# Kernel tuning notes

Measured on AMD Instinct MI355X. Metric: run time of the kernel, lower is better.

## Reference

```python
import jax, jax.numpy as jnp
import numpy as np

N = 50000
S = 32           # n_sample
D_IN = 256
D_OUT = 128
ALPHA = 0.2      # leakyrelu negative slope


def setup_inputs() -> dict:
    key = jax.random.key(0)
    k1, k2, k3, k4 = jax.random.split(key, 4)
    x = jax.random.normal(k1, (N, D_IN), dtype=jnp.float32)
    neibs = jax.random.randint(k2, (N, S), 0, N, dtype=jnp.int64)
    # xavier_uniform with gain=1.414
    limW = 1.414 * np.sqrt(6.0 / (D_IN + D_OUT))
    W = jax.random.uniform(k3, (D_IN, D_OUT), dtype=jnp.float32, minval=-limW, maxval=limW)
    lima = 1.414 * np.sqrt(6.0 / (2 * D_OUT + 1))
    a = jax.random.uniform(k4, (2 * D_OUT, 1), dtype=jnp.float32, minval=-lima, maxval=lima)
    return {"x": x, "neibs": neibs, "W": W, "a": a}


def reference(x, neibs, W, a):
    # x: [N, D_in], neibs: [N, S] int, W: [D_in, D_out], a: [2*D_out, 1]
    xw = x @ W                                  # [N, D_out]
    xn = xw[neibs]                              # [N, S, D_out] gathered neighbor feats
    # a_input @ a == xw @ a[:D_out] + xn @ a[D_out:]  (avoid materializing concat)
    a_self = a[:D_OUT, 0]                       # [D_out]
    a_neib = a[D_OUT:, 0]                       # [D_out]
    e = (xw @ a_self)[:, None] + jnp.einsum('nsd,d->ns', xn, a_neib)  # [N, S]
    e = jnp.where(e > 0, e, ALPHA * e)          # leakyrelu
    attention = jax.nn.softmax(e, axis=1)       # [N, S]  (dropout skipped: eval mode)
    h_prime = jnp.einsum('ns,nsd->nd', attention, xn)                # [N, D_out]
    output = jnp.concatenate([xw, h_prime], axis=1)                  # concat=True
    return jax.nn.elu(output)
```

## Files before the change

kernel.cpp:

```cpp
#include <hip/hip_runtime.h>
#include <math.h>

#define N_NODES 50000
#define S_NEIB 32
#define D_IN 256
#define D_OUT 128
#define ALPHA 0.2f

typedef __attribute__((ext_vector_type(8))) short bf16x8;
typedef __attribute__((ext_vector_type(4))) float f32x4;

__device__ __forceinline__ float elu_f(float v) {
    return v > 0.f ? v : (expf(v) - 1.f);
}

__device__ __forceinline__ unsigned short f2bf(float f) {
    unsigned u = __builtin_bit_cast(unsigned, f);
    u += 0x7fffu + ((u >> 16) & 1u);
    return (unsigned short)(u >> 16);
}

__global__ __launch_bounds__(256) void pack_w_kernel(
    const float* __restrict__ W, unsigned short* __restrict__ Wp)
{
    int tid = blockIdx.x * 256 + threadIdx.x;
    int j  = tid & 7;
    int t  = (tid >> 3) & 15;
    int kb = (tid >> 7) & 31;
    int c  = tid >> 12;
    Wp[tid] = f2bf(W[(kb * 8 + j) * D_OUT + c * 16 + t]);
}

__global__ __launch_bounds__(256) void gemm_score_kernel(
    const float* __restrict__ x, const unsigned short* __restrict__ Wp,
    const float* __restrict__ a, signed char* __restrict__ xq,
    float* __restrict__ rowscale,
    float* __restrict__ s_self, float* __restrict__ s_neib,
    float* __restrict__ out)
{
    __shared__ unsigned short xs[64 * 264];
    __shared__ float ps[2][4][64];
    __shared__ float psm[4][64];
    __shared__ float invs[64];

    const int tid  = threadIdx.x;
    const int lane = tid & 63;
    const int wave = tid >> 6;
    const int q    = lane >> 4;
    const int t    = lane & 15;
    const int colW = wave * 32;
    const int r0   = blockIdx.x * 64;

    for (int i = 0; i < 16; ++i) {
        int f4  = i * 256 + tid;
        int row = f4 >> 6;
        int c4  = (f4 & 63) << 2;
        float4 v = make_float4(0.f, 0.f, 0.f, 0.f);
        if (r0 + row < N_NODES)
            v = *(const float4*)(x + (size_t)(r0 + row) * D_IN + c4);
        ushort4 b;
        b.x = f2bf(v.x); b.y = f2bf(v.y); b.z = f2bf(v.z); b.w = f2bf(v.w);
        *(ushort4*)&xs[row * 264 + c4] = b;
    }
    __syncthreads();

    const bf16x8* Wp8 = (const bf16x8*)Wp;

    f32x4 acc[4][2];
    #pragma unroll
    for (int mt = 0; mt < 4; ++mt)
        #pragma unroll
        for (int nt = 0; nt < 2; ++nt)
            acc[mt][nt] = (f32x4){0.f, 0.f, 0.f, 0.f};

    #pragma unroll
    for (int kc = 0; kc < 8; ++kc) {
        const int k0 = kc * 32 + q * 8;
        bf16x8 afrag[4];
        #pragma unroll
        for (int mt = 0; mt < 4; ++mt)
            afrag[mt] = *(const bf16x8*)&xs[(mt * 16 + t) * 264 + k0];
        bf16x8 bfrag[2];
        #pragma unroll
        for (int nt = 0; nt < 2; ++nt)
            bfrag[nt] = Wp8[((wave * 2 + nt) * 32 + kc * 4 + q) * 16 + t];
        #pragma unroll
        for (int mt = 0; mt < 4; ++mt)
            #pragma unroll
            for (int nt = 0; nt < 2; ++nt)
                acc[mt][nt] = __builtin_amdgcn_mfma_f32_16x16x32_bf16(
                    afrag[mt], bfrag[nt], acc[mt][nt], 0, 0, 0);
    }

    const float as0 = a[colW + t],         as1 = a[colW + 16 + t];
    const float an0 = a[D_OUT + colW + t], an1 = a[D_OUT + colW + 16 + t];
    #pragma unroll
    for (int mt = 0; mt < 4; ++mt) {
        #pragma unroll
        for (int r = 0; r < 4; ++r) {
            float vs = acc[mt][0][r] * as0 + acc[mt][1][r] * as1;
            float vn = acc[mt][0][r] * an0 + acc[mt][1][r] * an1;
            float mv = fmaxf(fabsf(acc[mt][0][r]), fabsf(acc[mt][1][r]));
            #pragma unroll
            for (int d = 8; d >= 1; d >>= 1) {
                vs += __shfl_xor(vs, d);
                vn += __shfl_xor(vn, d);
                mv = fmaxf(mv, __shfl_xor(mv, d));
            }
            if (t == 0) {
                int row = mt * 16 + q * 4 + r;
                ps[0][wave][row] = vs;
                ps[1][wave][row] = vn;
                psm[wave][row]   = mv;
            }
        }
    }
    __syncthreads();
    if (tid < 64) {
        float rm = fmaxf(fmaxf(psm[0][tid], psm[1][tid]),
                         fmaxf(psm[2][tid], psm[3][tid]));
        rm = fmaxf(rm, 1e-20f);
        invs[tid] = 127.f / rm;
        if (r0 + tid < N_NODES) {
            rowscale[r0 + tid] = rm * (1.f / 127.f);
            s_self[r0 + tid] = ps[0][0][tid] + ps[0][1][tid] + ps[0][2][tid] + ps[0][3][tid];
            s_neib[r0 + tid] = ps[1][0][tid] + ps[1][1][tid] + ps[1][2][tid] + ps[1][3][tid];
        }
    }
    __syncthreads();

    #pragma unroll
    for (int mt = 0; mt < 4; ++mt) {
        #pragma unroll
        for (int r = 0; r < 4; ++r) {
            int row = mt * 16 + q * 4 + r;
            int g   = r0 + row;
            if (g < N_NODES) {
                float inv = invs[row];
                #pragma unroll
                for (int nt = 0; nt < 2; ++nt) {
                    int col = colW + nt * 16 + t;
                    float v = acc[mt][nt][r];
                    out[(size_t)g * (2 * D_OUT) + col] = elu_f(v);
                    float qf = fminf(fmaxf(rintf(v * inv), -127.f), 127.f);
                    xq[(size_t)g * D_OUT + col] = (signed char)(int)qf;
                }
            }
        }
    }
}

__global__ __launch_bounds__(256, 4) void aggregate_kernel(
    const int* __restrict__ neibs, const signed char* __restrict__ xq,
    const float* __restrict__ rowscale,
    const float* __restrict__ s_self, const float* __restrict__ s_neib,
    float* __restrict__ out)
{
    const int lane  = threadIdx.x & 63;
    const int wavei = threadIdx.x >> 6;
    const int n0 = (blockIdx.x * 4 + wavei) * 2;
    if (n0 >= N_NODES) return;

    const int half = lane >> 5;
    const int hl   = lane & 31;
    const int node = n0 + half;
    const int srcb = lane & 32;

    int   idx = neibs[n0 * S_NEIB + lane];
    float e   = s_self[node] + s_neib[idx];
    e = e > 0.f ? e : ALPHA * e;

    float m = e;
    #pragma unroll
    for (int d = 16; d >= 1; d >>= 1) m = fmaxf(m, __shfl_xor(m, d));
    float p = __expf(e - m);
    float ssum = p;
    #pragma unroll
    for (int d = 16; d >= 1; d >>= 1) ssum += __shfl_xor(ssum, d);
    float wj = (p / ssum) * rowscale[idx];

    const signed char* colp = xq + 4 * hl;

    float a0 = 0.f, a1 = 0.f, a2 = 0.f, a3 = 0.f;
    unsigned cur[8], nxt[8];

    #pragma unroll
    for (int i = 0; i < 8; ++i) {
        int j = __shfl(idx, srcb + i);
        cur[i] = *(const unsigned*)(colp + (size_t)j * D_OUT);
    }
    #pragma unroll
    for (int b = 0; b < 4; ++b) {
        if (b < 3) {
            #pragma unroll
            for (int i = 0; i < 8; ++i) {
                int j = __shfl(idx, srcb + (b + 1) * 8 + i);
                nxt[i] = *(const unsigned*)(colp + (size_t)j * D_OUT);
            }
        }
        #pragma unroll
        for (int i = 0; i < 8; ++i) {
            float w = __shfl(wj, srcb + b * 8 + i);
            unsigned v = cur[i];
            a0 = fmaf(w, (float)((int)(v << 24) >> 24), a0);
            a1 = fmaf(w, (float)((int)(v << 16) >> 24), a1);
            a2 = fmaf(w, (float)((int)(v <<  8) >> 24), a2);
            a3 = fmaf(w, (float)((int)v >> 24),         a3);
        }
        #pragma unroll
        for (int i = 0; i < 8; ++i) cur[i] = nxt[i];
    }

    float4 o;
    o.x = elu_f(a0);
    o.y = elu_f(a1);
    o.z = elu_f(a2);
    o.w = elu_f(a3);
    *(float4*)(out + (size_t)node * (2 * D_OUT) + D_OUT + 4 * hl) = o;
}

extern "C" void kernel_launch(void* const* d_in, const int* in_sizes, int n_in,
                              void* d_out, int out_size, void* d_ws, size_t ws_size,
                              hipStream_t stream) {
    const float* x     = (const float*)d_in[0];
    const int*   neibs = (const int*)  d_in[1];
    const float* W     = (const float*)d_in[2];
    const float* a     = (const float*)d_in[3];
    float* out = (float*)d_out;

    signed char* xq    = (signed char*)d_ws;
    float* rowscale    = (float*)(xq + (size_t)N_NODES * D_OUT);
    float* s_self      = rowscale + N_NODES;
    float* s_neib      = s_self + N_NODES;
    unsigned short* Wp = (unsigned short*)(s_neib + N_NODES);

    pack_w_kernel<<<128, 256, 0, stream>>>(W, Wp);
    gemm_score_kernel<<<(N_NODES + 63) / 64, 256, 0, stream>>>(
        x, Wp, a, xq, rowscale, s_self, s_neib, out);
    aggregate_kernel<<<(N_NODES + 7) / 8, 256, 0, stream>>>(
        neibs, xq, rowscale, s_self, s_neib, out);
}
```

Before: 154.1 us.

## Load GEMM A-fragments directly from global and split int8 quantization into separate kernel

The GEMM kernel no longer stages x through LDS. Each lane loads its A fragment straight from global memory and converts it to bf16, and the tile shrinks to 32 rows per block so occupancy can rise. The per-row max/quantization step moves out of the GEMM into a new quant_kernel that reads a bf16 copy of xw, which removes a block-wide reduction and a barrier from the GEMM. In exchange the change adds a bf16 write and read of xw, plus another launch. The row scale now comes from bf16-rounded values, which may change quantization slightly.

```diff
diff --git a/kernel.cpp b/kernel.cpp
--- a/kernel.cpp
+++ b/kernel.cpp
@@ -18,6 +18,15 @@
     unsigned u = __builtin_bit_cast(unsigned, f);
     u += 0x7fffu + ((u >> 16) & 1u);
     return (unsigned short)(u >> 16);
+}
+
+__device__ __forceinline__ bf16x8 pack_bf16x8(float4 v0, float4 v1) {
+    bf16x8 r;
+    r[0] = (short)f2bf(v0.x); r[1] = (short)f2bf(v0.y);
+    r[2] = (short)f2bf(v0.z); r[3] = (short)f2bf(v0.w);
+    r[4] = (short)f2bf(v1.x); r[5] = (short)f2bf(v1.y);
+    r[6] = (short)f2bf(v1.z); r[7] = (short)f2bf(v1.w);
+    return r;
 }
 
 __global__ __launch_bounds__(256) void pack_w_kernel(
@@ -31,17 +40,13 @@
     Wp[tid] = f2bf(W[(kb * 8 + j) * D_OUT + c * 16 + t]);
 }
 
-__global__ __launch_bounds__(256) void gemm_score_kernel(
+__global__ __launch_bounds__(256, 4) void gemm_score_kernel(
     const float* __restrict__ x, const unsigned short* __restrict__ Wp,
-    const float* __restrict__ a, signed char* __restrict__ xq,
-    float* __restrict__ rowscale,
+    const float* __restrict__ a, unsigned short* __restrict__ xwb,
     float* __restrict__ s_self, float* __restrict__ s_neib,
     float* __restrict__ out)
 {
-    __shared__ unsigned short xs[64 * 264];
-    __shared__ float ps[2][4][64];
-    __shared__ float psm[4][64];
-    __shared__ float invs[64];
+    __shared__ float ps[2][4][32];
 
     const int tid  = threadIdx.x;
     const int lane = tid & 63;
@@ -49,26 +54,17 @@
     const int q    = lane >> 4;
     const int t    = lane & 15;
     const int colW = wave * 32;
-    const int r0   = blockIdx.x * 64;
-
-    for (int i = 0; i < 16; ++i) {
-        int f4  = i * 256 + tid;
-        int row = f4 >> 6;
-        int c4  = (f4 & 63) << 2;
-        float4 v = make_float4(0.f, 0.f, 0.f, 0.f);
-        if (r0 + row < N_NODES)
-            v = *(const float4*)(x + (size_t)(r0 + row) * D_IN + c4);
-        ushort4 b;
-        b.x = f2bf(v.x); b.y = f2bf(v.y); b.z = f2bf(v.z); b.w = f2bf(v.w);
-        *(ushort4*)&xs[row * 264 + c4] = b;
-    }
-    __syncthreads();
+    const int r0   = blockIdx.x * 32;
+
+    int rowA[2];
+    rowA[0] = min(r0 + t,      N_NODES - 1);
+    rowA[1] = min(r0 + 16 + t, N_NODES - 1);
 
     const bf16x8* Wp8 = (const bf16x8*)Wp;
 
-    f32x4 acc[4][2];
-    #pragma unroll
-    for (int mt = 0; mt < 4; ++mt)
+    f32x4 acc[2][2];
+    #pragma unroll
+    for (int mt = 0; mt < 2; ++mt)
         #pragma unroll
         for (int nt = 0; nt < 2; ++nt)
             acc[mt][nt] = (f32x4){0.f, 0.f, 0.f, 0.f};
@@ -76,16 +72,20 @@
     #pragma unroll
     for (int kc = 0; kc < 8; ++kc) {
         const int k0 = kc * 32 + q * 8;
-        bf16x8 afrag[4];
-        #pragma unroll
-        for (int mt = 0; mt < 4; ++mt)
-            afrag[mt] = *(const bf16x8*)&xs[(mt * 16 + t) * 264 + k0];
+        bf16x8 afrag[2];
+        #pragma unroll
+        for (int mt = 0; mt < 2; ++mt) {
+            const float* xp = x + (size_t)rowA[mt] * D_IN + k0;
+            float4 v0 = *(const float4*)xp;
+            float4 v1 = *(const float4*)(xp + 4);
+            afrag[mt] = pack_bf16x8(v0, v1);
+        }
         bf16x8 bfrag[2];
         #pragma unroll
         for (int nt = 0; nt < 2; ++nt)
             bfrag[nt] = Wp8[((wave * 2 + nt) * 32 + kc * 4 + q) * 16 + t];
         #pragma unroll
-        for (int mt = 0; mt < 4; ++mt)
+        for (int mt = 0; mt < 2; ++mt)
             #pragma unroll
             for (int nt = 0; nt < 2; ++nt)
                 acc[mt][nt] = __builtin_amdgcn_mfma_f32_16x16x32_bf16(
@@ -95,58 +95,71 @@
     const float as0 = a[colW + t],         as1 = a[colW + 16 + t];
     const float an0 = a[D_OUT + colW + t], an1 = a[D_OUT + colW + 16 + t];
     #pragma unroll
-    for (int mt = 0; mt < 4; ++mt) {
+    for (int mt = 0; mt < 2; ++mt) {
         #pragma unroll
         for (int r = 0; r < 4; ++r) {
             float vs = acc[mt][0][r] * as0 + acc[mt][1][r] * as1;
             float vn = acc[mt][0][r] * an0 + acc[mt][1][r] * an1;
-            float mv = fmaxf(fabsf(acc[mt][0][r]), fabsf(acc[mt][1][r]));
             #pragma unroll
             for (int d = 8; d >= 1; d >>= 1) {
                 vs += __shfl_xor(vs, d);
                 vn += __shfl_xor(vn, d);
-                mv = fmaxf(mv, __shfl_xor(mv, d));
             }
             if (t == 0) {
                 int row = mt * 16 + q * 4 + r;
                 ps[0][wave][row] = vs;
                 ps[1][wave][row] = vn;
-                psm[wave][row]   = mv;
             }
         }
     }
     __syncthreads();
-    if (tid < 64) {
-        float rm = fmaxf(fmaxf(psm[0][tid], psm[1][tid]),
-                         fmaxf(psm[2][tid], psm[3][tid]));
-        rm = fmaxf(rm, 1e-20f);
-        invs[tid] = 127.f / rm;
-        if (r0 + tid < N_NODES) {
-            rowscale[r0 + tid] = rm * (1.f / 127.f);
-            s_self[r0 + tid] = ps[0][0][tid] + ps[0][1][tid] + ps[0][2][tid] + ps[0][3][tid];
-            s_neib[r0 + tid] = ps[1][0][tid] + ps[1][1][tid] + ps[1][2][tid] + ps[1][3][tid];
-        }
-    }
-    __syncthreads();
-
-    #pragma unroll
-    for (int mt = 0; mt < 4; ++mt) {
+    if (tid < 32 && r0 + tid < N_NODES) {
+        s_self[r0 + tid] = ps[0][0][tid] + ps[0][1][tid] + ps[0][2][tid] + ps[0][3][tid];
+        s_neib[r0 + tid] = ps[1][0][tid] + ps[1][1][tid] + ps[1][2][tid] + ps[1][3][tid];
+    }
+
+    #pragma unroll
+    for (int mt = 0; mt < 2; ++mt) {
         #pragma unroll
         for (int r = 0; r < 4; ++r) {
-            int row = mt * 16 + q * 4 + r;
-            int g   = r0 + row;
+            int g = r0 + mt * 16 + q * 4 + r;
             if (g < N_NODES) {
-                float inv = invs[row];
                 #pragma unroll
                 for (int nt = 0; nt < 2; ++nt) {
                     int col = colW + nt * 16 + t;
                     float v = acc[mt][nt][r];
+                    xwb[(size_t)g * D_OUT + col] = f2bf(v);
                     out[(size_t)g * (2 * D_OUT) + col] = elu_f(v);
-                    float qf = fminf(fmaxf(rintf(v * inv), -127.f), 127.f);
-                    xq[(size_t)g * D_OUT + col] = (signed char)(int)qf;
                 }
             }
         }
+    }
+}
+
+__global__ __launch_bounds__(256) void quant_kernel(
+    const unsigned short* __restrict__ xwb, signed char* __restrict__ xq,
+    float* __restrict__ rowscale)
+{
+    const int lane = threadIdx.x & 63;
+    const int wave = threadIdx.x >> 6;
+    #pragma unroll
+    for (int i = 0; i < 8; ++i) {
+        int r = blockIdx.x * 32 + wave * 8 + i;
+        if (r >= N_NODES) continue;
+        unsigned u = *(const unsigned*)(xwb + (size_t)r * D_OUT + 2 * lane);
+        unsigned ab = u & 0x7fff7fffu;
+        unsigned mb = max(ab >> 16, ab & 0xffffu);
+        #pragma unroll
+        for (int d = 32; d >= 1; d >>= 1) mb = max(mb, (unsigned)__shfl_xor((int)mb, d));
+        float scale = __builtin_bit_cast(float, mb << 16);
+        float inv = 127.f / fmaxf(scale, 1e-30f);
+        float flo = __builtin_bit_cast(float, u << 16);
+        float fhi = __builtin_bit_cast(float, u & 0xffff0000u);
+        int qlo = (int)rintf(flo * inv);
+        int qhi = (int)rintf(fhi * inv);
+        unsigned short pk = (unsigned short)((qlo & 0xff) | ((qhi & 0xff) << 8));
+        *(unsigned short*)(xq + (size_t)r * D_OUT + 2 * lane) = pk;
+        if (lane == 0) rowscale[r] = scale * (1.f / 127.f);
     }
 }
 
@@ -228,15 +241,17 @@
     const float* a     = (const float*)d_in[3];
     float* out = (float*)d_out;
 
-    signed char* xq    = (signed char*)d_ws;
-    float* rowscale    = (float*)(xq + (size_t)N_NODES * D_OUT);
-    float* s_self      = rowscale + N_NODES;
-    float* s_neib      = s_self + N_NODES;
-    unsigned short* Wp = (unsigned short*)(s_neib + N_NODES);
+    unsigned short* xwb = (unsigned short*)d_ws;
+    signed char* xq     = (signed char*)(xwb + (size_t)N_NODES * D_OUT);
+    float* rowscale     = (float*)(xq + (size_t)N_NODES * D_OUT);
+    float* s_self       = rowscale + N_NODES;
+    float* s_neib       = s_self + N_NODES;
+    unsigned short* Wp  = (unsigned short*)(s_neib + N_NODES);
 
     pack_w_kernel<<<128, 256, 0, stream>>>(W, Wp);
-    gemm_score_kernel<<<(N_NODES + 63) / 64, 256, 0, stream>>>(
-        x, Wp, a, xq, rowscale, s_self, s_neib, out);
+    gemm_score_kernel<<<(N_NODES + 31) / 32, 256, 0, stream>>>(
+        x, Wp, a, xwb, s_self, s_neib, out);
+    quant_kernel<<<(N_NODES + 31) / 32, 256, 0, stream>>>(xwb, xq, rowscale);
     aggregate_kernel<<<(N_NODES + 7) / 8, 256, 0, stream>>>(
         neibs, xq, rowscale, s_self, s_neib, out);
 }
```

Measured after the change: 171.7 us. 1.11x slower.
